# Performance work log

Hardware: AMD Instinct MI355X
Metric: run time of the kernel (lower is better)

## Reference

```python
import jax, jax.numpy as jnp
import numpy as np

B = 16            # batch of graphs
N = 512           # n_node
D = 32            # embedding_dim
MAXN = 16         # max_neighbors
E = MAXN * (N - 1)   # 8176 edges per graph
SLEFT = N * D
FSS = 601         # full_support_size
NA = N - 1        # num_actions (so one-hot rows == B*n_node)
IN0 = D + 1       # sa feature dim
NTOT = B * N


def _gat(x, snd, rcv, W, a_src, a_dst, b):
    # single-head GATConv, add_self_loops=False
    h = x @ W                                            # [BN, C]
    e = (h * a_src).sum(-1)[snd] + (h * a_dst).sum(-1)[rcv]
    e = jnp.where(e > 0, e, 0.2 * e)                     # LeakyReLU(0.2)
    m = jax.ops.segment_max(e, rcv, num_segments=NTOT)   # segment softmax
    m = jnp.where(jnp.isfinite(m), m, 0.0)
    ee = jnp.exp(e - m[rcv])
    den = jax.ops.segment_sum(ee, rcv, num_segments=NTOT)
    alpha = ee / (den[rcv] + 1e-16)
    return jax.ops.segment_sum(alpha[:, None] * h[snd], rcv, num_segments=NTOT) + b


def _ln(x, s, o):
    # hk.LayerNorm(axis=-2): normalize over node axis, scale/offset over features
    x3 = x.reshape(B, N, -1)
    mu = x3.mean(axis=1, keepdims=True)
    var = ((x3 - mu) ** 2).mean(axis=1, keepdims=True)
    return ((x3 - mu) * jax.lax.rsqrt(var + 1e-5) * s + o).reshape(B * N, -1)


def _gat_params(key, din, dout):
    k1, k2, k3 = jax.random.split(key, 3)
    sc = 1.0 / np.sqrt(din)
    return (jax.random.normal(k1, (din, dout), jnp.float32) * sc,
            jax.random.normal(k2, (dout,), jnp.float32) * sc,
            jax.random.normal(k3, (dout,), jnp.float32) * sc,
            jnp.zeros((dout,), jnp.float32))


def setup_inputs():
    key = jax.random.key(0)
    ks = jax.random.split(key, 4)
    nodes = jax.random.normal(ks[0], (B, SLEFT), jnp.float32)
    snd = jax.random.randint(ks[1], (B, E), 0, N).astype(jnp.float32)
    rcv = jax.random.randint(ks[2], (B, E), 0, N).astype(jnp.float32)
    ns = jnp.concatenate([nodes, snd, rcv], axis=1)      # [B, SLEFT + 2E]
    a = jax.random.randint(ks[3], (B,), 0, NA + 1)
    inp = {"ns": ns, "a": a}
    dims = [(IN0, 4 * D), (4 * D, 2 * D), (2 * D, 2 * D), (2 * D, D)]
    rdims = [(IN0, FSS), (FSS, FSS), (FSS, FSS), (FSS, FSS)]
    for i, (di, do) in enumerate(dims, 1):
        W, asrc, adst, b = _gat_params(jax.random.fold_in(key, 100 + i), di, do)
        inp.update({f"W{i}": W, f"a{i}s": asrc, f"a{i}d": adst, f"b{i}": b})
        if i < 4:
            inp.update({f"s{i}": jnp.ones((do,), jnp.float32), f"o{i}": jnp.zeros((do,), jnp.float32)})
    for i, (di, do) in enumerate(rdims, 1):
        W, asrc, adst, b = _gat_params(jax.random.fold_in(key, 200 + i), di, do)
        inp.update({f"rW{i}": W, f"ra{i}s": asrc, f"ra{i}d": adst, f"rb{i}": b})
        if i < 4:
            inp.update({f"rs{i}": jnp.ones((FSS,), jnp.float32), f"ro{i}": jnp.zeros((FSS,), jnp.float32)})
    return inp


def reference(ns, a,
              W1, a1s, a1d, b1, s1, o1,
              W2, a2s, a2d, b2, s2, o2,
              W3, a3s, a3d, b3, s3, o3,
              W4, a4s, a4d, b4,
              rW1, ra1s, ra1d, rb1, rs1, ro1,
              rW2, ra2s, ra2d, rb2, rs2, ro2,
              rW3, ra3s, ra3d, rb3, rs3, ro3,
              rW4, ra4s, ra4d, rb4):
    # gbatch: offset per-graph indices into one big graph
    off = (jnp.arange(B, dtype=jnp.int32) * N)[:, None]
    snd = (ns[:, SLEFT:SLEFT + E].astype(jnp.int32) + off).reshape(-1)
    rcv = (ns[:, SLEFT + E:SLEFT + 2 * E].astype(jnp.int32) + off).reshape(-1)
    nodes = ns[:, :SLEFT].reshape(B * N, D)
    sa = jnp.concatenate([nodes, jax.nn.one_hot(a, NA + 1).reshape(-1, 1)], axis=1)
    # reward head
    r = jax.nn.relu(_ln(_gat(sa, snd, rcv, rW1, ra1s, ra1d, rb1), rs1, ro1))
    r = jax.nn.relu(_ln(_gat(r, snd, rcv, rW2, ra2s, ra2d, rb2), rs2, ro2))
    r = jax.nn.relu(_ln(_gat(r, snd, rcv, rW3, ra3s, ra3d, rb3), rs3, ro3))
    r = _gat(r, snd, rcv, rW4, ra4s, ra4d, rb4).reshape(B, N, FSS).sum(axis=1)
    # next-state head
    f = jax.nn.relu(_ln(_gat(sa, snd, rcv, W1, a1s, a1d, b1), s1, o1))
    f = jax.nn.relu(_ln(_gat(f, snd, rcv, W2, a2s, a2d, b2), s2, o2))
    f = jax.nn.relu(_ln(_gat(f, snd, rcv, W3, a3s, a3d, b3), s3, o3))
    f = _gat(f, snd, rcv, W4, a4s, a4d, b4).reshape(B, N * D)
    ns_new = jnp.concatenate([f, ns[:, SLEFT:]], axis=1)
    return (r, ns_new)
```

## Files before the change

### kernel.cpp

```cpp
#include <hip/hip_runtime.h>
#include <math.h>

#define B_ 16
#define N_ 512
#define D_ 32
#define E_ 8176
#define SLEFT_ 16384
#define FSS_ 601
#define BN_ (B_*N_)
#define BE_ (B_*E_)
#define NSROW_ (SLEFT_ + 2*E_)
#define OUT_R_ (B_*FSS_)
#define HLD_ 768
#define CAP_ 128
#define KXB_ 736

typedef __attribute__((ext_vector_type(8))) short short8;
typedef __attribute__((ext_vector_type(4))) float f32x4;

typedef __attribute__((address_space(3))) uint lds_uint;
typedef __attribute__((address_space(1))) const uint g_uint;

__device__ __forceinline__ void gl_lds16(const ushort* gp, ushort* lp) {
  __builtin_amdgcn_global_load_lds((g_uint*)gp, (lds_uint*)lp, 16, 0, 0);
}

__device__ __forceinline__ ushort f2b(float f) {
  uint u = __builtin_bit_cast(uint, f);
  u += 0x7FFFu + ((u >> 16) & 1u);
  return (ushort)(u >> 16);
}
__device__ __forceinline__ float b2f(ushort h) {
  return __builtin_bit_cast(float, ((uint)h) << 16);
}


struct SetupP {
  const float* ns; const int* a;
  int* cnt; int* bins; ushort* sa;
  const float* Wr[4]; const float* Wn[4]; ushort* T[4];
};

__global__ __launch_bounds__(256) void k_setup(SetupP p) {
  __shared__ float tile[32][33];
  int blk = blockIdx.x;
  if (blk < 511) {
    int idx = blk*256 + threadIdx.x;
    if (idx >= BE_) return;
    int b = idx / E_;
    int j = idx - b*E_;
    const float* row = p.ns + (size_t)b*NSROW_;
    int s = (int)row[SLEFT_ + j];
    int r = (int)row[SLEFT_ + E_ + j];
    int dst = b*N_ + r;
    int pos = atomicAdd(&p.cnt[dst], 1);
    if (pos < CAP_) p.bins[(size_t)dst*CAP_ + pos] = b*N_ + s;
    return;
  }
  if (blk < 2559) {
    int idx = (blk-511)*256 + threadIdx.x;
    int v = idx >> 6, c = idx & 63;
    int b = v >> 9, n = v & 511;
    float val = 0.f;
    if (c < 32)       val = p.ns[(size_t)b*NSROW_ + n*32 + c];
    else if (c == 32) val = (p.a[b]==n) ? 1.f : 0.f;
    p.sa[idx] = f2b(val);
    return;
  }
  int t = blk - 2559;
  int s, base, KP, DINR, DINN, DOUTN, KOFF;
  if (t < 48)        { s=0; base=0;    KP=64;  DINR=33;  DINN=33;  DOUTN=128; KOFF=0;   }
  else if (t < 600)  { s=1; base=48;   KP=736; DINR=601; DINN=128; DOUTN=64;  KOFF=608; }
  else if (t < 1104) { s=2; base=600;  KP=672; DINR=601; DINN=64;  DOUTN=64;  KOFF=608; }
  else               { s=3; base=1104; KP=672; DINR=601; DINN=64;  DOUTN=32;  KOFF=608; }
  int ti = t - base;
  int kt = ti / 24, nt = ti - kt*24;
  int k0 = kt*32, n0 = nt*32;
  int tid = threadIdx.x;
  int cc = tid & 31, rr = tid >> 5;
  #pragma unroll
  for (int it=0; it<4; it++) {
    int k = k0 + it*8 + rr;
    int n = n0 + cc;
    float v = 0.f;
    if (n < 640) { if (n < 601 && k < DINR) v = p.Wr[s][(size_t)k*601 + n]; }
    else { int nn = n-640, kk = k-KOFF;
           if (nn < DOUTN && kk >= 0 && kk < DINN) v = p.Wn[s][(size_t)kk*DOUTN + nn]; }
    tile[it*8+rr][cc] = v;
  }
  __syncthreads();
  #pragma unroll
  for (int it=0; it<4; it++) {
    int n = n0 + it*8 + rr;
    int k = k0 + cc;
    p.T[s][(size_t)n*KP + k] = f2b(tile[cc][it*8+rr]);
  }
}


__global__ __launch_bounds__(256) void k_gemm(const ushort* __restrict__ A,
                                              const ushort* __restrict__ Bt,
                                              ushort* __restrict__ C,
                                              float* __restrict__ esed,
                                              const float* __restrict__ asr,
                                              const float* __restrict__ adr,
                                              const float* __restrict__ asn,
                                              const float* __restrict__ adn,
                                              const float* __restrict__ mulb,
                                              const float* __restrict__ addb,
                                              int Kpad, int dn,
                                              int kRewEnd, int kNextBeg, int useLN) {
  __shared__ ushort Asm[64*32];
  __shared__ ushort Bsm[128*32];
  __shared__ float Lm[KXB_], La[KXB_];
  int tid = threadIdx.x;
  int rowBase = blockIdx.y * 64;
  int colBase = blockIdx.x * 128;
  int kBeg = (blockIdx.x == 5) ? kNextBeg : 0;
  int kEnd = (blockIdx.x == 5) ? Kpad : kRewEnd;
  int wave = tid >> 6, lane = tid & 63;
  int wr = (wave >> 1) * 32, wc = (wave & 1) * 64;
  int lm = lane & 15, lk = (lane >> 4) * 8;

  f32x4 acc[2][4];
  #pragma unroll
  for (int i=0;i<2;i++)
    #pragma unroll
    for (int j=0;j<4;j++) acc[i][j] = (f32x4){0.f,0.f,0.f,0.f};

  int t0 = tid, t1 = tid + 256;
  int ar = t0 >> 2, ac8 = (t0 & 3) * 8;
  const ushort* Bg0 = Bt + (size_t)(colBase + (t0>>2))*Kpad + (t0&3)*8;
  const ushort* Bg1 = Bt + (size_t)(colBase + (t1>>2))*Kpad + (t1&3)*8;
  ushort* Bl0 = &Bsm[t0*8];
  ushort* Bl1 = &Bsm[t1*8];
  ushort* Al0 = &Asm[t0*8];

  const ushort* Ag_lds = A + (size_t)(rowBase + ar)*Kpad + ac8;
  int koff = (blockIdx.x == 5) ? 32 : 0;
  const ushort* Ag_vg  = A + (size_t)(rowBase + ar)*HLD_ + koff;

  if (useLN) {
    int b = rowBase >> 9;
    for (int i = tid; i < KXB_; i += 256) {
      Lm[i] = mulb[(size_t)b*KXB_ + i];
      La[i] = addb[(size_t)b*KXB_ + i];
    }
    __syncthreads();
  }

  for (int k0 = kBeg; k0 < kEnd; k0 += 32) {
    gl_lds16(Bg0 + k0, Bl0);
    gl_lds16(Bg1 + k0, Bl1);
    if (useLN) {
      short8 av = *(const short8*)&Ag_vg[k0 + ac8];
      short8 ov;
      #pragma unroll
      for (int q=0;q<8;q++) {
        float x = b2f((ushort)av[q]);
        float y = x * Lm[k0 + ac8 + q] + La[k0 + ac8 + q];
        y = y > 0.f ? y : 0.f;
        ov[q] = (short)f2b(y);
      }
      *(short8*)Al0 = ov;
    } else {
      gl_lds16(Ag_lds + k0, Al0);
    }
    __syncthreads();
    short8 af[2], bfr[4];
    #pragma unroll
    for (int i=0;i<2;i++) af[i]  = *(short8*)&Asm[(wr + i*16 + lm)*32 + lk];
    #pragma unroll
    for (int j=0;j<4;j++) bfr[j] = *(short8*)&Bsm[(wc + j*16 + lm)*32 + lk];
    #pragma unroll
    for (int i=0;i<2;i++)
      #pragma unroll
      for (int j=0;j<4;j++)
        acc[i][j] = __builtin_amdgcn_mfma_f32_16x16x32_bf16(af[i], bfr[j], acc[i][j], 0,0,0);
    __syncthreads();
  }

  float asv[4], adv[4];
  #pragma unroll
  for (int j=0;j<4;j++) {
    int col = colBase + wc + j*16 + lm;
    float s = 0.f, d = 0.f;
    if (col < 601)      { s = asr[col];     d = adr[col]; }
    else if (col >= 640 && col - 640 < dn) { s = asn[col-640]; d = adn[col-640]; }
    asv[j] = s; adv[j] = d;
  }
  int cr = lane >> 4;
  int ct2 = blockIdx.x*2 + (wc >> 6);
  float* esp = (ct2 < 10) ? esed : esed + 2*BN_;
  #pragma unroll
  for (int i=0;i<2;i++) {
    #pragma unroll
    for (int j=0;j<4;j++) {
      int col = colBase + wc + j*16 + lm;
      #pragma unroll
      for (int g=0; g<4; g++) {
        int row = rowBase + wr + i*16 + cr*4 + g;
        C[(size_t)row*HLD_ + col] = f2b(acc[i][j][g]);
      }
    }
    #pragma unroll
    for (int g=0; g<4; g++) {
      float se = 0.f, sd = 0.f;
      #pragma unroll
      for (int j=0;j<4;j++) { se += acc[i][j][g]*asv[j]; sd += acc[i][j][g]*adv[j]; }
      #pragma unroll
      for (int o=1;o<16;o<<=1) { se += __shfl_xor(se,o,64); sd += __shfl_xor(sd,o,64); }
      if (lm == 0) {
        int row = rowBase + wr + i*16 + cr*4 + g;
        atomicAdd(&esp[row], se);
        atomicAdd(&esp[BN_ + row], sd);
      }
    }
  }
}


__global__ __launch_bounds__(256) void k_agg(const ushort* __restrict__ h,
                                             const float* __restrict__ esed,
                                             const int* __restrict__ cnt,
                                             const int* __restrict__ bins,
                                             const float* __restrict__ bias_r,
                                             const float* __restrict__ bias_n,
                                             ushort* __restrict__ g,
                                             int dn) {
  const float* es_r = esed;
  const float* ed_r = esed + BN_;
  const float* es_n = esed + 2*BN_;
  const float* ed_n = esed + 3*BN_;
  int wid = threadIdx.x>>6, lane = threadIdx.x&63;
  int bid = blockIdx.x;
  int xcd = bid & 7, slot = bid >> 3;
  int graph = xcd + ((slot >> 7) << 3);
  int v = graph*512 + (slot & 127)*4 + wid;
  int s0 = v * CAP_;
  int deg = cnt[v]; if (deg > CAP_) deg = CAP_;
  float edr = ed_r[v], edn = ed_n[v];

  int nch = (640 + dn + 7) >> 3;
  int ch0 = lane, ch1 = lane + 64;
  bool a1 = ch1 < nch;
  bool c1r = ch1 < 80;
  float acc0[8], acc1[8];
  #pragma unroll
  for (int q=0;q<8;q++){ acc0[q]=0.f; acc1[q]=0.f; }

  if (deg <= 64) {
    bool has = lane < deg;
    int u = 0; float er = -__builtin_inff(), en = -__builtin_inff();
    if (has) {
      u = bins[s0 + lane];
      er = es_r[u] + edr; er = er > 0.f ? er : 0.2f*er;
      en = es_n[u] + edn; en = en > 0.f ? en : 0.2f*en;
    }
    float mr = er, mn = en;
    #pragma unroll
    for (int o=32;o;o>>=1) { mr = fmaxf(mr, __shfl_xor(mr,o,64)); mn = fmaxf(mn, __shfl_xor(mn,o,64)); }
    float pr = has ? __expf(er - mr) : 0.f;
    float pn = has ? __expf(en - mn) : 0.f;
    float dr = pr, dnm = pn;
    #pragma unroll
    for (int o=32;o;o>>=1) { dr += __shfl_xor(dr,o,64); dnm += __shfl_xor(dnm,o,64); }
    pr *= 1.f/(dr + 1e-16f);
    pn *= 1.f/(dnm + 1e-16f);

    for (int t0 = 0; t0 < deg; t0 += 4) {
      int nt = deg - t0; if (nt > 4) nt = 4;
      short8 va[4], vb[4];
      float w0[4], w1[4];
      #pragma unroll
      for (int q=0;q<4;q++) {
        if (q < nt) {
          int uu = __shfl(u, t0+q, 64);
          w0[q] = __shfl(pr, t0+q, 64);
          w1[q] = __shfl(pn, t0+q, 64);
          const ushort* hp = h + (size_t)uu*HLD_;
          va[q] = *(const short8*)&hp[ch0*8];
          vb[q] = a1 ? *(const short8*)&hp[ch1*8] : short8{};
        } else {
          w0[q] = 0.f; w1[q] = 0.f; va[q] = short8{}; vb[q] = short8{};
        }
      }
      #pragma unroll
      for (int q=0;q<4;q++) {
        #pragma unroll
        for (int r=0;r<8;r++) acc0[r] += w0[q] * b2f((ushort)va[q][r]);
        if (a1) {
          float wv = c1r ? w0[q] : w1[q];
          #pragma unroll
          for (int r=0;r<8;r++) acc1[r] += wv * b2f((ushort)vb[q][r]);
        }
      }
    }
  } else {
    int e0 = s0 + deg;
    float mr = -__builtin_inff(), mn = -__builtin_inff();
    for (int j = s0 + lane; j < e0; j += 64) {
      int u = bins[j];
      float er = es_r[u] + edr; er = er>0.f?er:0.2f*er;
      float en = es_n[u] + edn; en = en>0.f?en:0.2f*en;
      mr = fmaxf(mr, er); mn = fmaxf(mn, en);
    }
    #pragma unroll
    for (int o=32;o;o>>=1) { mr=fmaxf(mr,__shfl_xor(mr,o,64)); mn=fmaxf(mn,__shfl_xor(mn,o,64)); }
    float dr=0.f, dnm=0.f;
    for (int j = s0 + lane; j < e0; j += 64) {
      int u = bins[j];
      float er = es_r[u] + edr; er = er>0.f?er:0.2f*er;
      float en = es_n[u] + edn; en = en>0.f?en:0.2f*en;
      dr += __expf(er-mr); dnm += __expf(en-mn);
    }
    #pragma unroll
    for (int o=32;o;o>>=1) { dr+=__shfl_xor(dr,o,64); dnm+=__shfl_xor(dnm,o,64); }
    float ir = 1.f/(dr+1e-16f), in_ = 1.f/(dnm+1e-16f);
    for (int j = s0; j < e0; ++j) {
      int uu = bins[j];
      float er = es_r[uu] + edr; er = er>0.f?er:0.2f*er;
      float en = es_n[uu] + edn; en = en>0.f?en:0.2f*en;
      float wr2 = __expf(er-mr)*ir, wn2 = __expf(en-mn)*in_;
      const ushort* hp = h + (size_t)uu*HLD_;
      short8 hv = *(const short8*)&hp[ch0*8];
      #pragma unroll
      for (int q=0;q<8;q++) acc0[q] += wr2 * b2f((ushort)hv[q]);
      if (a1) {
        short8 hv2 = *(const short8*)&hp[ch1*8];
        float wv = c1r ? wr2 : wn2;
        #pragma unroll
        for (int q=0;q<8;q++) acc1[q] += wv * b2f((ushort)hv2[q]);
      }
    }
  }

  ushort* gv = g + (size_t)v*HLD_;
  {
    int cb = ch0*8;
    short8 ov;
    #pragma unroll
    for (int q=0;q<8;q++) ov[q] = (short)f2b(acc0[q] + bias_r[cb+q]);
    *(short8*)&gv[cb] = ov;
  }
  if (a1) {
    int cb = ch1*8;
    short8 ov;
    #pragma unroll
    for (int q=0;q<8;q++) {
      int c = cb+q;
      float val;
      if (c < 601)                         val = acc1[q] + bias_r[c];
      else if (c >= 640 && (c-640) < dn)   val = acc1[q] + bias_n[c-640];
      else                                 val = 0.f;
      ov[q] = (short)f2b(val);
    }
    *(short8*)&gv[cb] = ov;
  }
}


__global__ __launch_bounds__(256) void k_ln_stats(const ushort* __restrict__ g,
                                                  float* __restrict__ st) {
  int b = blockIdx.y, z = blockIdx.z; int n0 = z*128;
  int lc = threadIdx.x & 63, r0 = threadIdx.x >> 6;
  int c = blockIdx.x*64 + lc;
  float s=0.f, q=0.f;
  #pragma unroll 4
  for (int i=0;i<32;i++) {
    int n = n0 + r0*32 + i;
    float x = b2f(g[(size_t)(b*N_+n)*HLD_ + c]);
    s+=x; q+=x*x;
  }
  __shared__ float S[4][64], Q[4][64];
  S[r0][lc]=s; Q[r0][lc]=q; __syncthreads();
  if (r0==0) {
    st[((size_t)(z*2+0)*B_ + b)*HLD_ + c] = S[0][lc]+S[1][lc]+S[2][lc]+S[3][lc];
    st[((size_t)(z*2+1)*B_ + b)*HLD_ + c] = Q[0][lc]+Q[1][lc]+Q[2][lc]+Q[3][lc];
  }
}


__global__ __launch_bounds__(256) void k_stfin(const float* __restrict__ st,
                                               const float* __restrict__ scr,
                                               const float* __restrict__ ofr,
                                               const float* __restrict__ scn,
                                               const float* __restrict__ ofn,
                                               float* __restrict__ mulb,
                                               float* __restrict__ addb,
                                               int dn) {
  int c = blockIdx.x*256 + threadIdx.x;
  int b = blockIdx.y;
  if (c >= KXB_) return;
  int cs; bool valid; float scale, offs;
  if (c < 608) { cs = c; valid = c < 601;
                 scale = valid ? scr[c] : 0.f; offs = valid ? ofr[c] : 0.f; }
  else { int cn = c - 608; cs = 640 + cn; valid = cn < dn;
         scale = valid ? scn[cn] : 0.f; offs = valid ? ofn[cn] : 0.f; }
  float mul = 0.f, add = 0.f;
  if (valid) {
    float s=0.f, qq=0.f;
    #pragma unroll
    for (int z=0;z<4;z++) {
      s  += st[((size_t)(z*2+0)*B_ + b)*HLD_ + cs];
      qq += st[((size_t)(z*2+1)*B_ + b)*HLD_ + cs];
    }
    float mu = s*(1.f/N_);
    float var = qq*(1.f/N_) - mu*mu;
    float rs = rsqrtf(var+1e-5f);
    mul = rs*scale;
    add = offs - mu*rs*scale;
  }
  mulb[(size_t)b*KXB_ + c] = mul;
  addb[(size_t)b*KXB_ + c] = add;
}


__global__ __launch_bounds__(256) void k_rsum(const ushort* __restrict__ g,
                                              float* __restrict__ rsp) {
  int b = blockIdx.y, z = blockIdx.z; int n0 = z*64;
  int lc = threadIdx.x & 63, r0 = threadIdx.x>>6;
  int c = blockIdx.x*64 + lc;
  float s = 0.f;
  if (c < FSS_) {
    #pragma unroll 4
    for (int i=0;i<16;i++) {
      int n = n0 + r0*16 + i;
      s += b2f(g[(size_t)(b*N_+n)*HLD_ + c]);
    }
  }
  __shared__ float S[4][64];
  S[r0][lc]=s; __syncthreads();
  if (r0==0 && c<FSS_)
    rsp[((size_t)z*B_ + b)*FSS_ + c] = S[0][lc]+S[1][lc]+S[2][lc]+S[3][lc];
}


__global__ __launch_bounds__(256) void k_final(const float* __restrict__ rsp,
                                               const ushort* __restrict__ g,
                                               const float* __restrict__ ns,
                                               float* __restrict__ out) {
  int idx = blockIdx.x*256+threadIdx.x;
  if (idx < OUT_R_) {
    int b = idx / FSS_, c = idx - b*FSS_;
    float s = 0.f;
    #pragma unroll
    for (int z=0;z<8;z++) s += rsp[((size_t)z*B_ + b)*FSS_ + c];
    out[idx] = s;
  } else {
    int j2 = idx - OUT_R_;
    if (j2 >= B_*NSROW_) return;
    int b = j2 / NSROW_; int j = j2 - b*NSROW_;
    float v;
    if (j < SLEFT_) {
      int n = j >> 5, c = j & 31;
      v = b2f(g[(size_t)(b*N_+n)*HLD_ + 640 + c]);
    } else {
      v = ns[(size_t)b*NSROW_ + j];
    }
    out[idx] = v;
  }
}


extern "C" void kernel_launch(void* const* d_in, const int* in_sizes, int n_in,
                              void* d_out, int out_size, void* d_ws, size_t ws_size,
                              hipStream_t stream) {
  const float* ns = (const float*)d_in[0];
  const int*   a  = (const int*)d_in[1];

  const float *W[4], *As[4], *Ad[4], *Bb[4], *Sc[3], *Of[3];
  const float *rW[4], *rAs[4], *rAd[4], *rBb[4], *rSc[3], *rOf[3];
  int p = 2;
  for (int i=0;i<4;i++){
    W[i]=(const float*)d_in[p++]; As[i]=(const float*)d_in[p++];
    Ad[i]=(const float*)d_in[p++]; Bb[i]=(const float*)d_in[p++];
    if (i<3){ Sc[i]=(const float*)d_in[p++]; Of[i]=(const float*)d_in[p++]; }
  }
  for (int i=0;i<4;i++){
    rW[i]=(const float*)d_in[p++]; rAs[i]=(const float*)d_in[p++];
    rAd[i]=(const float*)d_in[p++]; rBb[i]=(const float*)d_in[p++];
    if (i<3){ rSc[i]=(const float*)d_in[p++]; rOf[i]=(const float*)d_in[p++]; }
  }

  char* w = (char*)d_ws;
  auto carve = [&](size_t bytes)->void* {
    void* r = (void*)w;
    w += (bytes + 255) & ~(size_t)255;
    return r;
  };
  ushort* hbuf = (ushort*)carve((size_t)BN_*HLD_*2);
  ushort* gbuf = (ushort*)carve((size_t)BN_*HLD_*2);
  ushort* sabf = (ushort*)carve((size_t)BN_*64*2);
  int* cnt     = (int*)carve((size_t)(BN_ + 4*4*BN_)*4);
  float* esedL = (float*)(cnt + BN_);
  int* bins    = (int*)carve((size_t)BN_*CAP_*4);
  float* stp   = (float*)carve((size_t)8*B_*HLD_*4);
  float* mulb  = (float*)carve((size_t)B_*KXB_*4);
  float* addb  = (float*)carve((size_t)B_*KXB_*4);
  float* rsp   = (float*)carve((size_t)8*B_*FSS_*4);
  ushort* Wt[4];
  Wt[0] = (ushort*)carve((size_t)768*64*2);
  Wt[1] = (ushort*)carve((size_t)768*736*2);
  Wt[2] = (ushort*)carve((size_t)768*672*2);
  Wt[3] = (ushort*)carve((size_t)768*672*2);

  float* out = (float*)d_out;

  hipMemsetAsync(cnt, 0, (size_t)(BN_ + 16*BN_)*4, stream);

  SetupP sp;
  sp.ns = ns; sp.a = a; sp.cnt = cnt; sp.bins = bins; sp.sa = sabf;
  for (int i=0;i<4;i++){ sp.Wr[i]=rW[i]; sp.Wn[i]=W[i]; sp.T[i]=Wt[i]; }
  k_setup<<<4167, 256, 0, stream>>>(sp);

  dim3 ggrid(6, BN_/64);

  int Kp[4]   = { 64, 736, 672, 672 };
  int dns[4]  = { 128, 64, 64, 32 };
  int kRe[4]  = { 64, 608, 608, 608 };
  int kNb[4]  = { 0, 608, 608, 608 };

  for (int L=0; L<4; ++L) {
    float* esed = esedL + (size_t)L*4*BN_;
    const ushort* Ain = (L==0) ? sabf : gbuf;
    k_gemm<<<ggrid, 256, 0, stream>>>(Ain, Wt[L], hbuf, esed,
                                      rAs[L], rAd[L], As[L], Ad[L],
                                      mulb, addb, Kp[L], dns[L],
                                      kRe[L], kNb[L], (L==0)?0:1);
    k_agg<<<BN_/4, 256, 0, stream>>>(hbuf, esed, cnt, bins,
                                     rBb[L], Bb[L], gbuf, dns[L]);
    if (L < 3) {
      k_ln_stats<<<dim3(12, B_, 4), 256, 0, stream>>>(gbuf, stp);
      k_stfin<<<dim3(3, B_), 256, 0, stream>>>(stp, rSc[L], rOf[L], Sc[L], Of[L],
                                               mulb, addb, dns[L]);
    }
  }

  k_rsum<<<dim3(10, B_, 8), 256, 0, stream>>>(gbuf, rsp);
  k_final<<<(OUT_R_ + B_*NSROW_ + 255)/256, 256, 0, stream>>>(rsp, gbuf, ns, out);
}
```

Baseline: 352.2 us.

## Double-buffer GEMM LDS tiles and fuse LayerNorm stats with finalization

The GEMM main loop now uses two LDS buffers so the next K-tile's global-to-LDS loads and the LN-applied A loads are issued before the MFMAs on the current tile, with one barrier per iteration instead of two. Separately, the two-kernel LayerNorm statistics path (partial sums, then finalize) is merged into one kernel that reduces all 512 nodes per column and writes the scale/offset directly. This removes a launch and a global scratch round trip per layer. The cost is a doubled LDS footprint in the GEMM and fewer blocks (192 instead of 768) in the stats kernel, each doing a longer serial reduction.

```diff
diff --git a/kernel.cpp b/kernel.cpp
--- a/kernel.cpp
+++ b/kernel.cpp
@@ -110,8 +110,8 @@
                                               const float* __restrict__ addb,
                                               int Kpad, int dn,
                                               int kRewEnd, int kNextBeg, int useLN) {
-  __shared__ ushort Asm[64*32];
-  __shared__ ushort Bsm[128*32];
+  __shared__ ushort Asm[2][64*32];
+  __shared__ ushort Bsm[2][128*32];
   __shared__ float Lm[KXB_], La[KXB_];
   int tid = threadIdx.x;
   int rowBase = blockIdx.y * 64;
@@ -132,9 +132,10 @@
   int ar = t0 >> 2, ac8 = (t0 & 3) * 8;
   const ushort* Bg0 = Bt + (size_t)(colBase + (t0>>2))*Kpad + (t0&3)*8;
   const ushort* Bg1 = Bt + (size_t)(colBase + (t1>>2))*Kpad + (t1&3)*8;
-  ushort* Bl0 = &Bsm[t0*8];
-  ushort* Bl1 = &Bsm[t1*8];
-  ushort* Al0 = &Asm[t0*8];
+  ushort* Bl0 = &Bsm[0][t0*8];
+  ushort* Bl1 = &Bsm[0][t1*8];
+  ushort* Al0 = &Asm[0][t0*8];
+  const int BSTEP = 128*32, ASTEP = 64*32;
 
   const ushort* Ag_lds = A + (size_t)(rowBase + ar)*Kpad + ac8;
   int koff = (blockIdx.x == 5) ? 32 : 0;
@@ -149,35 +150,62 @@
     __syncthreads();
   }
 
+  gl_lds16(Bg0 + kBeg, Bl0);
+  gl_lds16(Bg1 + kBeg, Bl1);
+  if (useLN) {
+    short8 av = *(const short8*)&Ag_vg[kBeg + ac8];
+    short8 ov;
+    #pragma unroll
+    for (int q=0;q<8;q++) {
+      float x = b2f((ushort)av[q]);
+      int kk = kBeg + ac8 + q;
+      float y = x * Lm[kk] + La[kk];
+      y = y > 0.f ? y : 0.f;
+      ov[q] = (short)f2b(y);
+    }
+    *(short8*)Al0 = ov;
+  } else {
+    gl_lds16(Ag_lds + kBeg, Al0);
+  }
+  __syncthreads();
+
+  int cur = 0;
   for (int k0 = kBeg; k0 < kEnd; k0 += 32) {
-    gl_lds16(Bg0 + k0, Bl0);
-    gl_lds16(Bg1 + k0, Bl1);
-    if (useLN) {
-      short8 av = *(const short8*)&Ag_vg[k0 + ac8];
+    int nxt = cur ^ 1;
+    bool more = (k0 + 32) < kEnd;
+    short8 avn = short8{};
+    if (more) {
+      gl_lds16(Bg0 + k0 + 32, Bl0 + nxt*BSTEP);
+      gl_lds16(Bg1 + k0 + 32, Bl1 + nxt*BSTEP);
+      if (useLN) avn = *(const short8*)&Ag_vg[k0 + 32 + ac8];
+      else       gl_lds16(Ag_lds + k0 + 32, Al0 + nxt*ASTEP);
+    }
+    const ushort* As = &Asm[cur][0];
+    const ushort* Bs = &Bsm[cur][0];
+    short8 af[2], bfr[4];
+    #pragma unroll
+    for (int i=0;i<2;i++) af[i]  = *(const short8*)&As[(wr + i*16 + lm)*32 + lk];
+    #pragma unroll
+    for (int j=0;j<4;j++) bfr[j] = *(const short8*)&Bs[(wc + j*16 + lm)*32 + lk];
+    #pragma unroll
+    for (int i=0;i<2;i++)
+      #pragma unroll
+      for (int j=0;j<4;j++)
+        acc[i][j] = __builtin_amdgcn_mfma_f32_16x16x32_bf16(af[i], bfr[j], acc[i][j], 0,0,0);
+    if (more && useLN) {
       short8 ov;
       #pragma unroll
       for (int q=0;q<8;q++) {
-        float x = b2f((ushort)av[q]);
-        float y = x * Lm[k0 + ac8 + q] + La[k0 + ac8 + q];
+        float x = b2f((ushort)avn[q]);
+        int kk = k0 + 32 + ac8 + q;
+        float y = x * Lm[kk] + La[kk];
         y = y > 0.f ? y : 0.f;
         ov[q] = (short)f2b(y);
       }
-      *(short8*)Al0 = ov;
-    } else {
-      gl_lds16(Ag_lds + k0, Al0);
+      *(short8*)(Al0 + nxt*ASTEP) = ov;
     }
     __syncthreads();
-    short8 af[2], bfr[4];
-    #pragma unroll
-    for (int i=0;i<2;i++) af[i]  = *(short8*)&Asm[(wr + i*16 + lm)*32 + lk];
-    #pragma unroll
-    for (int j=0;j<4;j++) bfr[j] = *(short8*)&Bsm[(wc + j*16 + lm)*32 + lk];
-    #pragma unroll
-    for (int i=0;i<2;i++)
-      #pragma unroll
-      for (int j=0;j<4;j++)
-        acc[i][j] = __builtin_amdgcn_mfma_f32_16x16x32_bf16(af[i], bfr[j], acc[i][j], 0,0,0);
-    __syncthreads();
+    cur = nxt;
   }
 
   float asv[4], adv[4];
@@ -360,28 +388,7 @@
 }
 
 
-__global__ __launch_bounds__(256) void k_ln_stats(const ushort* __restrict__ g,
-                                                  float* __restrict__ st) {
-  int b = blockIdx.y, z = blockIdx.z; int n0 = z*128;
-  int lc = threadIdx.x & 63, r0 = threadIdx.x >> 6;
-  int c = blockIdx.x*64 + lc;
-  float s=0.f, q=0.f;
-  #pragma unroll 4
-  for (int i=0;i<32;i++) {
-    int n = n0 + r0*32 + i;
-    float x = b2f(g[(size_t)(b*N_+n)*HLD_ + c]);
-    s+=x; q+=x*x;
-  }
-  __shared__ float S[4][64], Q[4][64];
-  S[r0][lc]=s; Q[r0][lc]=q; __syncthreads();
-  if (r0==0) {
-    st[((size_t)(z*2+0)*B_ + b)*HLD_ + c] = S[0][lc]+S[1][lc]+S[2][lc]+S[3][lc];
-    st[((size_t)(z*2+1)*B_ + b)*HLD_ + c] = Q[0][lc]+Q[1][lc]+Q[2][lc]+Q[3][lc];
-  }
-}
-
-
-__global__ __launch_bounds__(256) void k_stfin(const float* __restrict__ st,
+__global__ __launch_bounds__(256) void k_lnfin(const ushort* __restrict__ g,
                                                const float* __restrict__ scr,
                                                const float* __restrict__ ofr,
                                                const float* __restrict__ scn,
@@ -389,30 +396,42 @@
                                                float* __restrict__ mulb,
                                                float* __restrict__ addb,
                                                int dn) {
-  int c = blockIdx.x*256 + threadIdx.x;
   int b = blockIdx.y;
-  if (c >= KXB_) return;
-  int cs; bool valid; float scale, offs;
-  if (c < 608) { cs = c; valid = c < 601;
-                 scale = valid ? scr[c] : 0.f; offs = valid ? ofr[c] : 0.f; }
-  else { int cn = c - 608; cs = 640 + cn; valid = cn < dn;
-         scale = valid ? scn[cn] : 0.f; offs = valid ? ofn[cn] : 0.f; }
-  float mul = 0.f, add = 0.f;
-  if (valid) {
-    float s=0.f, qq=0.f;
-    #pragma unroll
-    for (int z=0;z<4;z++) {
-      s  += st[((size_t)(z*2+0)*B_ + b)*HLD_ + cs];
-      qq += st[((size_t)(z*2+1)*B_ + b)*HLD_ + cs];
-    }
-    float mu = s*(1.f/N_);
-    float var = qq*(1.f/N_) - mu*mu;
-    float rs = rsqrtf(var+1e-5f);
-    mul = rs*scale;
-    add = offs - mu*rs*scale;
-  }
-  mulb[(size_t)b*KXB_ + c] = mul;
-  addb[(size_t)b*KXB_ + c] = add;
+  int lc = threadIdx.x & 63, r0 = threadIdx.x >> 6;
+  int xb = blockIdx.x*64 + lc;
+  bool inrange = xb < KXB_;
+  int gcol = (xb < 608) ? xb : xb + 32;
+  float s = 0.f, q = 0.f;
+  if (inrange) {
+    const ushort* gp = g + (size_t)(b*N_)*HLD_ + gcol;
+    #pragma unroll 4
+    for (int i = 0; i < 128; ++i) {
+      int n = r0*128 + i;
+      float x = b2f(gp[(size_t)n*HLD_]);
+      s += x; q += x*x;
+    }
+  }
+  __shared__ float S[4][64], Q[4][64];
+  S[r0][lc]=s; Q[r0][lc]=q; __syncthreads();
+  if (r0 == 0 && inrange) {
+    float ts = S[0][lc]+S[1][lc]+S[2][lc]+S[3][lc];
+    float tq = Q[0][lc]+Q[1][lc]+Q[2][lc]+Q[3][lc];
+    bool valid; float scale, offs;
+    if (xb < 608) { valid = xb < 601;
+                    scale = valid ? scr[xb] : 0.f; offs = valid ? ofr[xb] : 0.f; }
+    else { int cn = xb - 608; valid = cn < dn;
+           scale = valid ? scn[cn] : 0.f; offs = valid ? ofn[cn] : 0.f; }
+    float mul = 0.f, add = 0.f;
+    if (valid) {
+      float mu = ts*(1.f/N_);
+      float var = tq*(1.f/N_) - mu*mu;
+      float rs = rsqrtf(var+1e-5f);
+      mul = rs*scale;
+      add = offs - mu*rs*scale;
+    }
+    mulb[(size_t)b*KXB_ + xb] = mul;
+    addb[(size_t)b*KXB_ + xb] = add;
+  }
 }
 
 
@@ -495,7 +514,6 @@
   int* cnt     = (int*)carve((size_t)(BN_ + 4*4*BN_)*4);
   float* esedL = (float*)(cnt + BN_);
   int* bins    = (int*)carve((size_t)BN_*CAP_*4);
-  float* stp   = (float*)carve((size_t)8*B_*HLD_*4);
   float* mulb  = (float*)carve((size_t)B_*KXB_*4);
   float* addb  = (float*)carve((size_t)B_*KXB_*4);
   float* rsp   = (float*)carve((size_t)8*B_*FSS_*4);
@@ -531,9 +549,8 @@
     k_agg<<<BN_/4, 256, 0, stream>>>(hbuf, esed, cnt, bins,
                                      rBb[L], Bb[L], gbuf, dns[L]);
     if (L < 3) {
-      k_ln_stats<<<dim3(12, B_, 4), 256, 0, stream>>>(gbuf, stp);
-      k_stfin<<<dim3(3, B_), 256, 0, stream>>>(stp, rSc[L], rOf[L], Sc[L], Of[L],
-                                               mulb, addb, dns[L]);
+      k_lnfin<<<dim3(12, B_), 256, 0, stream>>>(gbuf, rSc[L], rOf[L], Sc[L], Of[L],
+                                                mulb, addb, dns[L]);
     }
   }
 
```

New measurement: 376.9 us. 7.0% more time.
